# Kernel optimization log

Measured on AMD Instinct MI355X. Metric: run time of the kernel, lower is better.

## Reference

```python
import jax, jax.numpy as jnp
import numpy as np

N_WAY, K_SHOT = 5, 1
N_CLASSES = 64
D = 8


def _conv(x, w, b):
    y = jax.lax.conv_general_dilated(x, w, (2, 2), 'SAME',
                                     dimension_numbers=('NCHW', 'OIHW', 'NCHW'))
    return jax.nn.relu(y + b[None, :, None, None])


def setup_inputs() -> dict:
    key = jax.random.key(0)
    ks = jax.random.split(key, 12)
    b, s_sup, q, h, w = 4, N_WAY * K_SHOT, 1, 64, 64
    rnd = lambda k, shape: jax.random.normal(k, shape, jnp.float32) * 0.05
    return {
        'support_x': jax.random.normal(ks[0], (b, s_sup, 3, h, w), jnp.float32),
        'support_y': jax.random.randint(ks[1], (b, s_sup), 0, N_CLASSES),
        'query_x': jax.random.normal(ks[2], (b, q, 3, h, w), jnp.float32),
        'query_y': jax.random.randint(ks[3], (b, q), 0, N_CLASSES),
        'k1': rnd(ks[4], (32, 3, 3, 3)), 'bc1': jnp.zeros((32,), jnp.float32),
        'k2': rnd(ks[5], (48, 32, 3, 3)), 'bc2': jnp.zeros((48,), jnp.float32),
        'k3': rnd(ks[6], (64, 48, 3, 3)), 'bc3': jnp.zeros((64,), jnp.float32),
        'Wlog': rnd(ks[7], (64, N_CLASSES)), 'blog': jnp.zeros((N_CLASSES,), jnp.float32),
        'Wg1': rnd(ks[8], (132, 128)), 'bg1': jnp.zeros((128,), jnp.float32),
        'Wg2': rnd(ks[9], (128, 64)), 'bg2': jnp.zeros((64,), jnp.float32),
        'Wf1': rnd(ks[10], (64, 16)), 'bf1': jnp.zeros((16,), jnp.float32),
        'Wf2': rnd(ks[11], (16, 1)), 'bf2': jnp.zeros((1,), jnp.float32),
    }


def reference(support_x, support_y, query_x, query_y,
              k1, bc1, k2, bc2, k3, bc3, Wlog, blog,
              Wg1, bg1, Wg2, bg2, Wf1, bf1, Wf2, bf2):
    x = jnp.concatenate([support_x, query_x], axis=1)       # [b, s, 3, h, w]
    label = jnp.concatenate([support_y, query_y], axis=1)   # [b, s]
    b, s = label.shape
    h, w = x.shape[-2:]

    feat = x.reshape(b * s, 3, h, w)
    feat = _conv(feat, k1, bc1)
    feat = _conv(feat, k2, bc2)
    feat = _conv(feat, k3, bc3)                              # [b*s, c, D, D]
    c = feat.shape[1]
    logits = feat.mean(axis=(2, 3)) @ Wlog + blog            # [b*s, n_classes]

    # --- append normalized (i/d, j/d) coord channels ---
    ii = jnp.arange(D, dtype=feat.dtype) / D
    coord = jnp.stack([jnp.broadcast_to(ii[:, None], (D, D)),
                       jnp.broadcast_to(ii[None, :], (D, D))])        # [2, D, D]
    feat = feat.reshape(b, s, c, D, D)
    feat = jnp.concatenate([feat, jnp.broadcast_to(coord, (b, s, 2, D, D))], axis=2)
    c2 = c + 2
    m = D * D
    a = feat.reshape(b, s, c2, m).transpose(0, 1, 3, 2)      # [b, s, m, c2]

    # --- relation network g over all (set-pair, position-pair) combos ---
    # original: g(concat(x_i, x_j)) where x_i = x[b, j, :, q], x_j = x[b, i, :, p]
    # split first linear: concat @ Wg1 = x_i @ Wg1[:c2] + x_j @ Wg1[c2:]
    W1a, W1b = Wg1[:c2], Wg1[c2:]
    u = a @ W1a                                              # [b, s_j, m_q, 128]
    v = a @ W1b + bg1                                        # [b, s_i, m_p, 128]
    # hdd[b,i,j,q,p] = relu(u[b,j,q] + v[b,i,p])  -> [b, s, s, m, m, 128]
    hdd = jax.nn.relu(u[:, None, :, :, None, :] + v[:, :, None, None, :, :])
    g = jax.nn.relu(hdd @ Wg2 + bg2)                         # [b, s, s, m, m, 64]
    x_f = g.sum(axis=(3, 4))                                 # [b, s, s, 64]
    score = jax.nn.sigmoid(jax.nn.relu(x_f @ Wf1 + bf1) @ Wf2 + bf2)  # [b, s, s, 1]

    # --- losses ---
    logp = jax.nn.log_softmax(logits, axis=-1)
    lab = label.reshape(-1)
    cls_loss = -jnp.take_along_axis(logp, lab[:, None], axis=1).mean()

    y = (label[:, :, None] == label[:, None, :])[..., None].astype(score.dtype)
    P = score[..., 0]                                        # [b, s, s]
    Pt = P.transpose(0, 2, 1)
    sym, anti = 0.5 * (P + Pt), 0.5 * (P - Pt)
    sym_n = jnp.sqrt((sym ** 2).sum(axis=(1, 2)))            # Frobenius per batch
    anti_n = jnp.sqrt((anti ** 2).sum(axis=(1, 2)))
    sym_loss = ((sym_n - anti_n) / (sym_n + anti_n)).mean()
    euc_loss = ((score - y) ** 2).mean()
    rn_loss = euc_loss - 0.1 * sym_loss
    return (cls_loss, rn_loss, sym_loss)
```

## Files before the change

### kernel.cpp

```cpp
#include <hip/hip_runtime.h>

typedef _Float16 f16x8 __attribute__((ext_vector_type(8)));
typedef float f32x4 __attribute__((ext_vector_type(4)));

__device__ unsigned g_rel_done = 0;


__global__ void __launch_bounds__(256) conv1_k(
        const float* __restrict__ sx, const float* __restrict__ qx,
        const float* __restrict__ w, const float* __restrict__ bias,
        float* __restrict__ out,
        const float* __restrict__ Wg2, _Float16* __restrict__ W2h) {
    if (blockIdx.x == 768) {
        for (int s = 0; s < 4; s++) {
            int slot = threadIdx.x + 256*s;
            int tile = slot >> 6, lane = slot & 63;
            int kt = tile >> 2, nt = tile & 3;
            int quad = lane >> 4, col = lane & 15;
            f16x8 t;
            #pragma unroll
            for (int jj = 0; jj < 8; jj++)
                t[jj] = (_Float16)Wg2[(kt*32 + quad*8 + jj)*64 + nt*16 + col];
            *(f16x8*)&W2h[slot*8] = t;
        }
        return;
    }
    int r8 = blockIdx.x & 7, q = blockIdx.x >> 3;
    int n  = (q >> 5)*8 + r8;
    int oc = q & 31;
    int bi = n / 6, si = n % 6;
    const float* inp = (si < 5) ? sx + (size_t)((bi*5+si)*3)*4096
                                : qx + (size_t)(bi*3)*4096;
    __shared__ __align__(16) float ish[3*4352];
    __shared__ float wl[27];
    __shared__ float bl;
    const int tid = threadIdx.x;
    #pragma unroll
    for (int j = 0; j < 12; j++) {
        int k = tid + j*256;
        f32x4 t = *(const f32x4*)&inp[k*4];
        int plane = k >> 10, rem = k & 1023, row = rem >> 4, c4 = (rem & 15)*4;
        *(f32x4*)&ish[plane*4352 + row*68 + c4] = t;
    }
    if (tid < 27) wl[tid] = w[oc*27 + tid];
    if (tid == 31) bl = bias[oc];
    __syncthreads();
    for (int idx = tid; idx < 1024; idx += 256) {
        int oy = idx >> 5, ox = idx & 31;
        float acc = bl;
        #pragma unroll
        for (int ic = 0; ic < 3; ic++) {
            const float* ip = &ish[ic*4352];
            #pragma unroll
            for (int dy = 0; dy < 3; dy++) {
                int iy = 2*oy + dy;
                if (iy >= 64) continue;
                #pragma unroll
                for (int dx = 0; dx < 3; dx++) {
                    int ix = 2*ox + dx;
                    if (ix >= 64) continue;
                    acc += ip[iy*68+ix] * wl[ic*9 + dy*3 + dx];
                }
            }
        }
        out[(size_t)(n*32+oc)*1024 + idx] = fmaxf(acc, 0.f);
    }
}

__global__ void __launch_bounds__(256) conv2_k(
        const float* __restrict__ in, const float* __restrict__ w,
        const float* __restrict__ bias, float* __restrict__ out) {
    int r8 = blockIdx.x & 7, q = blockIdx.x >> 3;
    int n   = (q / 12)*8 + r8;
    int ocg = q % 12;
    __shared__ __align__(16) float wl[1152];
    __shared__ __align__(16) float pin[16*1152];
    const int tid = threadIdx.x;
    const float* ib = in + (size_t)n*32*1024;
    #pragma unroll
    for (int j = 0; j < 16; j++) {
        int k = tid + j*256;
        f32x4 t = *(const f32x4*)&ib[k*4];
        int s = k >> 8, rem = k & 255, row = rem >> 3, c4 = (rem & 7)*4;
        *(f32x4*)&pin[s*1152 + row*36 + c4] = t;
    }
    f32x4 rb[16];
    #pragma unroll
    for (int j = 0; j < 16; j++) {
        int k = tid + j*256;
        rb[j] = *(const f32x4*)&ib[16384 + k*4];
    }
    for (int e = tid; e < 288; e += 256)
        *(f32x4*)&wl[e*4] = *(const f32x4*)&w[ocg*1152 + e*4];
    __syncthreads();
    int oy = tid >> 4, ox = tid & 15;
    float a0 = bias[ocg*4+0], a1 = bias[ocg*4+1];
    float a2 = bias[ocg*4+2], a3 = bias[ocg*4+3];
    #pragma unroll 4
    for (int ic = 0; ic < 16; ic++) {
        const float* pp = &pin[ic*1152];
        float tap[9];
        #pragma unroll
        for (int dy = 0; dy < 3; dy++)
            #pragma unroll
            for (int dx = 0; dx < 3; dx++) {
                int iy = 2*oy+dy, ix = 2*ox+dx;
                tap[dy*3+dx] = (iy < 32 && ix < 32) ? pp[iy*36 + ix] : 0.f;
            }
        #pragma unroll
        for (int t = 0; t < 9; t++) {
            a0 += tap[t]*wl[0*288 + ic*9 + t];
            a1 += tap[t]*wl[1*288 + ic*9 + t];
            a2 += tap[t]*wl[2*288 + ic*9 + t];
            a3 += tap[t]*wl[3*288 + ic*9 + t];
        }
    }
    __syncthreads();
    #pragma unroll
    for (int j = 0; j < 16; j++) {
        int k = tid + j*256;
        int s = k >> 8, rem = k & 255, row = rem >> 3, c4 = (rem & 7)*4;
        *(f32x4*)&pin[s*1152 + row*36 + c4] = rb[j];
    }
    __syncthreads();
    #pragma unroll 4
    for (int ic = 16; ic < 32; ic++) {
        const float* pp = &pin[(ic-16)*1152];
        float tap[9];
        #pragma unroll
        for (int dy = 0; dy < 3; dy++)
            #pragma unroll
            for (int dx = 0; dx < 3; dx++) {
                int iy = 2*oy+dy, ix = 2*ox+dx;
                tap[dy*3+dx] = (iy < 32 && ix < 32) ? pp[iy*36 + ix] : 0.f;
            }
        #pragma unroll
        for (int t = 0; t < 9; t++) {
            a0 += tap[t]*wl[0*288 + ic*9 + t];
            a1 += tap[t]*wl[1*288 + ic*9 + t];
            a2 += tap[t]*wl[2*288 + ic*9 + t];
            a3 += tap[t]*wl[3*288 + ic*9 + t];
        }
    }
    size_t ob = (size_t)(n*48 + ocg*4)*256 + tid;
    out[ob        ] = fmaxf(a0, 0.f);
    out[ob + 256  ] = fmaxf(a1, 0.f);
    out[ob + 512  ] = fmaxf(a2, 0.f);
    out[ob + 768  ] = fmaxf(a3, 0.f);
}

__global__ void __launch_bounds__(256) conv3_k(
        const float* __restrict__ in, const float* __restrict__ w,
        const float* __restrict__ bias, float* __restrict__ out,
        float* __restrict__ mf) {
    int r8 = blockIdx.x & 7, q = blockIdx.x >> 3;
    int n   = (q >> 3)*8 + r8;
    int ocg = q & 7;
    __shared__ __align__(16) float wl[3456];
    __shared__ __align__(16) float pin[48*320];
    const int tid = threadIdx.x;
    const float* ib = in + (size_t)n*48*256;
    #pragma unroll
    for (int j = 0; j < 12; j++) {
        int k = tid + j*256;
        f32x4 t = *(const f32x4*)&ib[k*4];
        int plane = k >> 6, rem = k & 63, row = rem >> 2, c4 = (rem & 3)*4;
        *(f32x4*)&pin[plane*320 + row*20 + c4] = t;
    }
    for (int e = tid; e < 864; e += 256)
        *(f32x4*)&wl[e*4] = *(const f32x4*)&w[ocg*3456 + e*4];
    __syncthreads();
    int pix = tid & 63, osub = tid >> 6;
    int oy = pix >> 3, ox = pix & 7;
    int ol0 = osub*2;
    float a0 = bias[ocg*8 + ol0], a1 = bias[ocg*8 + ol0 + 1];
    #pragma unroll 4
    for (int ic = 0; ic < 48; ic++) {
        const float* pp = &pin[ic*320];
        float tap[9];
        #pragma unroll
        for (int dy = 0; dy < 3; dy++)
            #pragma unroll
            for (int dx = 0; dx < 3; dx++) {
                int iy = 2*oy+dy, ix = 2*ox+dx;
                tap[dy*3+dx] = (iy < 16 && ix < 16) ? pp[iy*20 + ix] : 0.f;
            }
        #pragma unroll
        for (int t = 0; t < 9; t++) {
            a0 += tap[t]*wl[ ol0   *432 + ic*9 + t];
            a1 += tap[t]*wl[(ol0+1)*432 + ic*9 + t];
        }
    }
    float r0 = fmaxf(a0, 0.f), r1 = fmaxf(a1, 0.f);
    out[(size_t)(n*64 + ocg*8 + ol0  )*64 + pix] = r0;
    out[(size_t)(n*64 + ocg*8 + ol0+1)*64 + pix] = r1;
    #pragma unroll
    for (int off = 32; off >= 1; off >>= 1) {
        r0 += __shfl_xor(r0, off, 64);
        r1 += __shfl_xor(r1, off, 64);
    }
    if (pix == 0) {
        mf[n*64 + ocg*8 + ol0    ] = r0 * (1.f/64.f);
        mf[n*64 + ocg*8 + ol0 + 1] = r1 * (1.f/64.f);
    }
}

__global__ void uvcls_k(const float* __restrict__ feat3, const float* __restrict__ Wg1,
                        const float* __restrict__ bg1, _Float16* __restrict__ u,
                        _Float16* __restrict__ v,
                        const float* __restrict__ mf, const int* __restrict__ sy,
                        const int* __restrict__ qy, const float* __restrict__ Wlog,
                        const float* __restrict__ blog, float* __restrict__ rv) {
    int tid = threadIdx.x;
    if (blockIdx.x >= 384) {
        int n = blockIdx.x - 384;
        if (tid >= 64) return;
        int lane = tid;
        float s = blog[lane];
        for (int c = 0; c < 64; c++) s += mf[n*64 + c] * Wlog[c*64 + lane];
        float mx = s;
        #pragma unroll
        for (int off = 32; off >= 1; off >>= 1) mx = fmaxf(mx, __shfl_xor(mx, off, 64));
        float p = __expf(s - mx);
        float se = p;
        #pragma unroll
        for (int off = 32; off >= 1; off >>= 1) se += __shfl_xor(se, off, 64);
        int bi = n/6, si = n%6;
        int lab = (si < 5) ? sy[bi*5+si] : qy[bi];
        float s_lab = __shfl(s, lab, 64);
        if (lane == 0) rv[n] = -(s_lab - mx - __logf(se));
        return;
    }
    int r8 = blockIdx.x & 7, q = blockIdx.x >> 3;
    int bs = (q >> 4)*8 + r8;
    int pg = q & 15;
    __shared__ float a4[4][66];
    for (int e = tid; e < 264; e += 128) {
        int pl = e / 66, c = e % 66;
        int p = pg*4 + pl;
        float vv;
        if (c < 64)       vv = feat3[(size_t)(bs*64 + c)*64 + p];
        else if (c == 64) vv = (float)(p >> 3) * 0.125f;
        else              vv = (float)(p & 7) * 0.125f;
        a4[pl][c] = vv;
    }
    __syncthreads();
    float us[4] = {0.f,0.f,0.f,0.f};
    float bg = bg1[tid];
    float vs[4] = {bg,bg,bg,bg};
    for (int c = 0; c < 66; c++) {
        float wa = Wg1[c*128 + tid];
        float wb = Wg1[(66+c)*128 + tid];
        #pragma unroll
        for (int pl = 0; pl < 4; pl++) {
            us[pl] += a4[pl][c]*wa;
            vs[pl] += a4[pl][c]*wb;
        }
    }
    #pragma unroll
    for (int pl = 0; pl < 4; pl++) {
        int p = pg*4 + pl;
        u[(size_t)(bs*64+p)*128 + tid] = (_Float16)us[pl];
        v[(size_t)(bs*64+p)*128 + tid] = (_Float16)vs[pl];
    }
}

__global__ void __launch_bounds__(256, 2) rel_k(
        const _Float16* __restrict__ U, const _Float16* __restrict__ V,
        const _Float16* __restrict__ W2h, const float* __restrict__ bg2,
        float* __restrict__ xfpT,
        const float* __restrict__ rv,
        const int* __restrict__ sy, const int* __restrict__ qy,
        const float* __restrict__ Wf1, const float* __restrict__ bf1,
        const float* __restrict__ Wf2, const float* __restrict__ bf2,
        float* __restrict__ out) {
    __shared__ __align__(16) float smem[1792];
    __shared__ unsigned lastflag;
    _Float16* Vsh   = (_Float16*)smem;
    float*    xfred = smem + 1024;

    int r8 = blockIdx.x & 7, qq = blockIdx.x >> 3;
    int b = r8 >> 1;
    int m = (qq << 1) | (r8 & 1);
    int cb = m >> 2, qc = m & 3;
    int j = cb / 6, i = cb % 6;
    int tid  = threadIdx.x;
    int wv   = tid >> 6, lane = tid & 63;
    int col  = lane & 15, quad = lane >> 4;

    const _Float16* ub = U + (size_t)(b*6 + i)*8192;
    const _Float16* vb = V + (size_t)(b*6 + j)*8192 + qc*16*128;

    *(f16x8*)&Vsh[tid*8] = *(const f16x8*)&vb[tid*8];

    f16x8 uf[4];
    {
        const _Float16* up = ub + (wv*16 + col)*128 + quad*8;
        #pragma unroll
        for (int kt = 0; kt < 4; kt++) uf[kt] = *(const f16x8*)&up[kt*32];
    }
    f16x8 bf[4][4];
    #pragma unroll
    for (int kt = 0; kt < 4; kt++)
        #pragma unroll
        for (int nt = 0; nt < 4; nt++)
            bf[kt][nt] = *(const f16x8*)&W2h[(size_t)(((kt*4+nt)*64) + lane)*8];
    float bgv[4];
    #pragma unroll
    for (int nt = 0; nt < 4; nt++) bgv[nt] = bg2[nt*16 + col];

    __syncthreads();

    float sums[4] = {0.f,0.f,0.f,0.f};
    for (int qi = 0; qi < 16; qi++) {
        const _Float16* vp = &Vsh[qi*128 + quad*8];
        f32x4 acc[4];
        #pragma unroll
        for (int nt = 0; nt < 4; nt++)
            acc[nt] = (f32x4){bgv[nt], bgv[nt], bgv[nt], bgv[nt]};
        #pragma unroll
        for (int kt = 0; kt < 4; kt++) {
            f16x8 vf = *(const f16x8*)&vp[kt*32];
            f16x8 af = uf[kt] + vf;
            af = __builtin_elementwise_max(af, (f16x8){0,0,0,0,0,0,0,0});
            #pragma unroll
            for (int nt = 0; nt < 4; nt++)
                acc[nt] = __builtin_amdgcn_mfma_f32_16x16x32_f16(af, bf[kt][nt], acc[nt], 0, 0, 0);
        }
        #pragma unroll
        for (int nt = 0; nt < 4; nt++)
            #pragma unroll
            for (int rr = 0; rr < 4; rr++)
                sums[nt] += fmaxf(acc[nt][rr], 0.f);
    }

    #pragma unroll
    for (int nt = 0; nt < 4; nt++) {
        sums[nt] += __shfl_xor(sums[nt], 16, 64);
        sums[nt] += __shfl_xor(sums[nt], 32, 64);
    }
    if (lane < 16) {
        #pragma unroll
        for (int nt = 0; nt < 4; nt++) xfred[wv*64 + nt*16 + lane] = sums[nt];
    }
    __syncthreads();
    if (tid < 64) {
        float val = xfred[tid] + xfred[64+tid] + xfred[128+tid] + xfred[192+tid];
        __hip_atomic_store(&xfpT[(size_t)tid*576 + (unsigned)(b*144 + m)], val,
                           __ATOMIC_RELAXED, __HIP_MEMORY_SCOPE_AGENT);
    }
    if (wv == 0) asm volatile("s_waitcnt vmcnt(0)" ::: "memory");
    if (tid == 0) {
        unsigned my = __hip_atomic_fetch_add(&g_rel_done, 1u, __ATOMIC_RELAXED,
                                             __HIP_MEMORY_SCOPE_AGENT);
        lastflag = ((my % 576u) == 575u) ? 1u : 0u;
    }
    __syncthreads();
    if (!lastflag) return;

    {
        float* Wf1sh = smem;
        float* wf2sh = smem + 1024;
        float* bf1sh = smem + 1040;
        float* Pm    = smem + 1056;
        int*   lab   = (int*)(smem + 1200);
        float* red   = smem + 1232;
        float* ratio = smem + 1488;
        for (int e = tid; e < 1024; e += 256) Wf1sh[e] = Wf1[e];
        if (tid < 16) { wf2sh[tid] = Wf2[tid]; bf1sh[tid] = bf1[tid]; }
        if (tid < 24) { int bi = tid/6, si = tid%6; lab[tid] = (si < 5) ? sy[bi*5+si] : qy[bi]; }
        __syncthreads();
        if (tid < 144) {
            float hid[16];
            #pragma unroll
            for (int h = 0; h < 16; h++) hid[h] = bf1sh[h];
            for (int nn = 0; nn < 64; nn++) {
                const float* xp = &xfpT[(size_t)nn*576 + tid*4];
                float x = 0.f;
                #pragma unroll
                for (int c = 0; c < 4; c++)
                    x += __hip_atomic_load(&xp[c], __ATOMIC_RELAXED,
                                           __HIP_MEMORY_SCOPE_AGENT);
                #pragma unroll
                for (int h = 0; h < 16; h++) hid[h] += x * Wf1sh[nn*16 + h];
            }
            float sc = bf2[0];
            #pragma unroll
            for (int h = 0; h < 16; h++) sc += fmaxf(hid[h], 0.f) * wf2sh[h];
            Pm[tid] = 1.f/(1.f + __expf(-sc));
        }
        __syncthreads();
        float e = 0.f;
        if (tid < 144) {
            int bb = tid/36, r = tid%36, jj = r/6, ii = r%6;
            float y = (lab[bb*6+jj] == lab[bb*6+ii]) ? 1.f : 0.f;
            float d = Pm[tid] - y;
            e = d*d;
        }
        red[tid] = e;
        __syncthreads();
        for (int s = 128; s > 0; s >>= 1) {
            if (tid < s) red[tid] += red[tid+s];
            __syncthreads();
        }
        if (tid < 4) {
            float s2 = 0.f, a2 = 0.f;
            for (int jj = 0; jj < 6; jj++)
                for (int ii = 0; ii < 6; ii++) {
                    float pa = Pm[tid*36 + jj*6 + ii], pb = Pm[tid*36 + ii*6 + jj];
                    float sm = 0.5f*(pa+pb), an = 0.5f*(pa-pb);
                    s2 += sm*sm; a2 += an*an;
                }
            float sn = sqrtf(s2), anq = sqrtf(a2);
            ratio[tid] = (sn - anq)/(sn + anq);
        }
        __syncthreads();
        if (tid == 0) {
            float sl = 0.25f*(ratio[0]+ratio[1]+ratio[2]+ratio[3]);
            float euc = red[0] * (1.f/144.f);
            float cs = 0.f;
            for (int k = 0; k < 24; k++) cs += rv[k];
            out[0] = cs * (1.f/24.f);
            out[1] = euc - 0.1f*sl;
            out[2] = sl;
        }
    }
}

extern "C" void kernel_launch(void* const* d_in, const int* in_sizes, int n_in,
                              void* d_out, int out_size, void* d_ws, size_t ws_size,
                              hipStream_t stream) {
    const float* sx   = (const float*)d_in[0];
    const int*   sy   = (const int*)  d_in[1];
    const float* qx   = (const float*)d_in[2];
    const int*   qy   = (const int*)  d_in[3];
    const float* k1   = (const float*)d_in[4];
    const float* bc1  = (const float*)d_in[5];
    const float* k2   = (const float*)d_in[6];
    const float* bc2  = (const float*)d_in[7];
    const float* k3   = (const float*)d_in[8];
    const float* bc3  = (const float*)d_in[9];
    const float* Wlog = (const float*)d_in[10];
    const float* blog = (const float*)d_in[11];
    const float* Wg1  = (const float*)d_in[12];
    const float* bg1  = (const float*)d_in[13];
    const float* Wg2  = (const float*)d_in[14];
    const float* bg2  = (const float*)d_in[15];
    const float* Wf1  = (const float*)d_in[16];
    const float* bf1  = (const float*)d_in[17];
    const float* Wf2  = (const float*)d_in[18];
    const float* bf2  = (const float*)d_in[19];

    float* ws    = (float*)d_ws;
    float* feat1 = ws;
    float* feat2 = feat1 + 786432;
    float* feat3 = feat2 + 294912;
    float* mf    = feat3 + 98304;
    float* rv    = mf    + 1536;
    float* xfpT  = rv    + 32;
    _Float16* u16 = (_Float16*)(xfpT + 36864);
    _Float16* v16 = u16 + 196608;
    _Float16* W2h = v16 + 196608;
    float* out   = (float*)d_out;

    conv1_k <<<769,    256, 0, stream>>>(sx, qx, k1, bc1, feat1, Wg2, W2h);
    conv2_k <<<24*12,  256, 0, stream>>>(feat1, k2, bc2, feat2);
    conv3_k <<<24*8,   256, 0, stream>>>(feat2, k3, bc3, feat3, mf);
    uvcls_k <<<408,    128, 0, stream>>>(feat3, Wg1, bg1, u16, v16,
                                         mf, sy, qy, Wlog, blog, rv);
    rel_k   <<<576,    256, 0, stream>>>(u16, v16, W2h, bg2, xfpT,
                                         rv, sy, qy, Wf1, bf1, Wf2, bf2, out);
}
```

Baseline: 162.8 us.

## Fuse conv2, conv3 and u/v projection into one kernel via last-block-per-image

Merges the conv2, conv3 and uv/classifier kernels into a single launch. Each of the 12 conv2 blocks for an image bumps a per-image atomic counter, and the last one to finish computes conv3, the mean features, the u/v projection and the classification loss for that image. This removes two kernel launches and the intermediate global round-trips between them. In exchange, conv3 and the u/v work now run serially on only 24 blocks, down from 192 and 408, which risks a long serialized tail.

```diff
diff --git a/kernel.cpp b/kernel.cpp
--- a/kernel.cpp
+++ b/kernel.cpp
@@ -4,6 +4,7 @@
 typedef float f32x4 __attribute__((ext_vector_type(4)));
 
 __device__ unsigned g_rel_done = 0;
+__device__ unsigned g_img_done[24] = {};
 
 
 __global__ void __launch_bounds__(256) conv1_k(
@@ -67,157 +68,206 @@
     }
 }
 
-__global__ void __launch_bounds__(256) conv2_k(
-        const float* __restrict__ in, const float* __restrict__ w,
-        const float* __restrict__ bias, float* __restrict__ out) {
+__global__ void __launch_bounds__(256) fused_k(
+        const float* __restrict__ feat1, const float* __restrict__ k2w,
+        const float* __restrict__ bc2, float* __restrict__ feat2,
+        const float* __restrict__ k3w, const float* __restrict__ bc3,
+        float* __restrict__ feat3g,
+        const float* __restrict__ Wg1, const float* __restrict__ bg1,
+        _Float16* __restrict__ u16, _Float16* __restrict__ v16,
+        const int* __restrict__ sy, const int* __restrict__ qy,
+        const float* __restrict__ Wlog, const float* __restrict__ blog,
+        float* __restrict__ rv) {
+    __shared__ __align__(16) float smem[19584];
+    __shared__ unsigned lastflag;
+    const int tid = threadIdx.x;
+
     int r8 = blockIdx.x & 7, q = blockIdx.x >> 3;
     int n   = (q / 12)*8 + r8;
     int ocg = q % 12;
-    __shared__ __align__(16) float wl[1152];
-    __shared__ __align__(16) float pin[16*1152];
-    const int tid = threadIdx.x;
-    const float* ib = in + (size_t)n*32*1024;
-    #pragma unroll
-    for (int j = 0; j < 16; j++) {
-        int k = tid + j*256;
-        f32x4 t = *(const f32x4*)&ib[k*4];
-        int s = k >> 8, rem = k & 255, row = rem >> 3, c4 = (rem & 7)*4;
-        *(f32x4*)&pin[s*1152 + row*36 + c4] = t;
-    }
-    f32x4 rb[16];
-    #pragma unroll
-    for (int j = 0; j < 16; j++) {
-        int k = tid + j*256;
-        rb[j] = *(const f32x4*)&ib[16384 + k*4];
-    }
-    for (int e = tid; e < 288; e += 256)
-        *(f32x4*)&wl[e*4] = *(const f32x4*)&w[ocg*1152 + e*4];
-    __syncthreads();
-    int oy = tid >> 4, ox = tid & 15;
-    float a0 = bias[ocg*4+0], a1 = bias[ocg*4+1];
-    float a2 = bias[ocg*4+2], a3 = bias[ocg*4+3];
-    #pragma unroll 4
-    for (int ic = 0; ic < 16; ic++) {
-        const float* pp = &pin[ic*1152];
-        float tap[9];
-        #pragma unroll
-        for (int dy = 0; dy < 3; dy++)
-            #pragma unroll
-            for (int dx = 0; dx < 3; dx++) {
-                int iy = 2*oy+dy, ix = 2*ox+dx;
-                tap[dy*3+dx] = (iy < 32 && ix < 32) ? pp[iy*36 + ix] : 0.f;
-            }
-        #pragma unroll
-        for (int t = 0; t < 9; t++) {
-            a0 += tap[t]*wl[0*288 + ic*9 + t];
-            a1 += tap[t]*wl[1*288 + ic*9 + t];
-            a2 += tap[t]*wl[2*288 + ic*9 + t];
-            a3 += tap[t]*wl[3*288 + ic*9 + t];
-        }
-    }
-    __syncthreads();
-    #pragma unroll
-    for (int j = 0; j < 16; j++) {
-        int k = tid + j*256;
-        int s = k >> 8, rem = k & 255, row = rem >> 3, c4 = (rem & 7)*4;
-        *(f32x4*)&pin[s*1152 + row*36 + c4] = rb[j];
-    }
-    __syncthreads();
-    #pragma unroll 4
-    for (int ic = 16; ic < 32; ic++) {
-        const float* pp = &pin[(ic-16)*1152];
-        float tap[9];
-        #pragma unroll
-        for (int dy = 0; dy < 3; dy++)
-            #pragma unroll
-            for (int dx = 0; dx < 3; dx++) {
-                int iy = 2*oy+dy, ix = 2*ox+dx;
-                tap[dy*3+dx] = (iy < 32 && ix < 32) ? pp[iy*36 + ix] : 0.f;
-            }
-        #pragma unroll
-        for (int t = 0; t < 9; t++) {
-            a0 += tap[t]*wl[0*288 + ic*9 + t];
-            a1 += tap[t]*wl[1*288 + ic*9 + t];
-            a2 += tap[t]*wl[2*288 + ic*9 + t];
-            a3 += tap[t]*wl[3*288 + ic*9 + t];
-        }
-    }
-    size_t ob = (size_t)(n*48 + ocg*4)*256 + tid;
-    out[ob        ] = fmaxf(a0, 0.f);
-    out[ob + 256  ] = fmaxf(a1, 0.f);
-    out[ob + 512  ] = fmaxf(a2, 0.f);
-    out[ob + 768  ] = fmaxf(a3, 0.f);
-}
-
-__global__ void __launch_bounds__(256) conv3_k(
-        const float* __restrict__ in, const float* __restrict__ w,
-        const float* __restrict__ bias, float* __restrict__ out,
-        float* __restrict__ mf) {
-    int r8 = blockIdx.x & 7, q = blockIdx.x >> 3;
-    int n   = (q >> 3)*8 + r8;
-    int ocg = q & 7;
-    __shared__ __align__(16) float wl[3456];
-    __shared__ __align__(16) float pin[48*320];
-    const int tid = threadIdx.x;
-    const float* ib = in + (size_t)n*48*256;
-    #pragma unroll
-    for (int j = 0; j < 12; j++) {
-        int k = tid + j*256;
-        f32x4 t = *(const f32x4*)&ib[k*4];
-        int plane = k >> 6, rem = k & 63, row = rem >> 2, c4 = (rem & 3)*4;
-        *(f32x4*)&pin[plane*320 + row*20 + c4] = t;
-    }
-    for (int e = tid; e < 864; e += 256)
-        *(f32x4*)&wl[e*4] = *(const f32x4*)&w[ocg*3456 + e*4];
-    __syncthreads();
+
+    {
+        float* wl  = smem;
+        float* pin = smem + 1152;
+        const float* ib = feat1 + (size_t)n*32*1024;
+        #pragma unroll
+        for (int j = 0; j < 16; j++) {
+            int k = tid + j*256;
+            f32x4 t = *(const f32x4*)&ib[k*4];
+            int s = k >> 8, rem = k & 255, row = rem >> 3, c4 = (rem & 7)*4;
+            *(f32x4*)&pin[s*1152 + row*36 + c4] = t;
+        }
+        f32x4 rb[16];
+        #pragma unroll
+        for (int j = 0; j < 16; j++) {
+            int k = tid + j*256;
+            rb[j] = *(const f32x4*)&ib[16384 + k*4];
+        }
+        for (int e = tid; e < 288; e += 256)
+            *(f32x4*)&wl[e*4] = *(const f32x4*)&k2w[ocg*1152 + e*4];
+        __syncthreads();
+        int oy = tid >> 4, ox = tid & 15;
+        float a0 = bc2[ocg*4+0], a1 = bc2[ocg*4+1];
+        float a2 = bc2[ocg*4+2], a3 = bc2[ocg*4+3];
+        #pragma unroll 4
+        for (int ic = 0; ic < 16; ic++) {
+            const float* pp = &pin[ic*1152];
+            float tap[9];
+            #pragma unroll
+            for (int dy = 0; dy < 3; dy++)
+                #pragma unroll
+                for (int dx = 0; dx < 3; dx++) {
+                    int iy = 2*oy+dy, ix = 2*ox+dx;
+                    tap[dy*3+dx] = (iy < 32 && ix < 32) ? pp[iy*36 + ix] : 0.f;
+                }
+            #pragma unroll
+            for (int t = 0; t < 9; t++) {
+                a0 += tap[t]*wl[0*288 + ic*9 + t];
+                a1 += tap[t]*wl[1*288 + ic*9 + t];
+                a2 += tap[t]*wl[2*288 + ic*9 + t];
+                a3 += tap[t]*wl[3*288 + ic*9 + t];
+            }
+        }
+        __syncthreads();
+        #pragma unroll
+        for (int j = 0; j < 16; j++) {
+            int k = tid + j*256;
+            int s = k >> 8, rem = k & 255, row = rem >> 3, c4 = (rem & 7)*4;
+            *(f32x4*)&pin[s*1152 + row*36 + c4] = rb[j];
+        }
+        __syncthreads();
+        #pragma unroll 4
+        for (int ic = 16; ic < 32; ic++) {
+            const float* pp = &pin[(ic-16)*1152];
+            float tap[9];
+            #pragma unroll
+            for (int dy = 0; dy < 3; dy++)
+                #pragma unroll
+                for (int dx = 0; dx < 3; dx++) {
+                    int iy = 2*oy+dy, ix = 2*ox+dx;
+                    tap[dy*3+dx] = (iy < 32 && ix < 32) ? pp[iy*36 + ix] : 0.f;
+                }
+            #pragma unroll
+            for (int t = 0; t < 9; t++) {
+                a0 += tap[t]*wl[0*288 + ic*9 + t];
+                a1 += tap[t]*wl[1*288 + ic*9 + t];
+                a2 += tap[t]*wl[2*288 + ic*9 + t];
+                a3 += tap[t]*wl[3*288 + ic*9 + t];
+            }
+        }
+        size_t ob = (size_t)(n*48 + ocg*4)*256 + tid;
+        __hip_atomic_store(&feat2[ob      ], fmaxf(a0, 0.f), __ATOMIC_RELAXED, __HIP_MEMORY_SCOPE_AGENT);
+        __hip_atomic_store(&feat2[ob + 256], fmaxf(a1, 0.f), __ATOMIC_RELAXED, __HIP_MEMORY_SCOPE_AGENT);
+        __hip_atomic_store(&feat2[ob + 512], fmaxf(a2, 0.f), __ATOMIC_RELAXED, __HIP_MEMORY_SCOPE_AGENT);
+        __hip_atomic_store(&feat2[ob + 768], fmaxf(a3, 0.f), __ATOMIC_RELAXED, __HIP_MEMORY_SCOPE_AGENT);
+    }
+    asm volatile("s_waitcnt vmcnt(0)" ::: "memory");
+    __syncthreads();
+    if (tid == 0) {
+        unsigned my = __hip_atomic_fetch_add(&g_img_done[n], 1u, __ATOMIC_RELAXED,
+                                             __HIP_MEMORY_SCOPE_AGENT);
+        lastflag = ((my % 12u) == 11u) ? 1u : 0u;
+    }
+    __syncthreads();
+    if (!lastflag) return;
+
+    float* pin3 = smem;
+    float* wl3  = smem + 15360;
+    float* mfsh = smem + 18816;
+    float* a4uv = smem + 18880;
+
+    {
+        const float* f2 = feat2 + (size_t)n*48*256;
+        #pragma unroll 8
+        for (int jj = 0; jj < 48; jj++) {
+            int k = tid + jj*256;
+            float vIn = __hip_atomic_load(&f2[k], __ATOMIC_RELAXED,
+                                          __HIP_MEMORY_SCOPE_AGENT);
+            int plane = k >> 8, rem = k & 255, row = rem >> 4, cc = rem & 15;
+            pin3[plane*320 + row*20 + cc] = vIn;
+        }
+    }
     int pix = tid & 63, osub = tid >> 6;
-    int oy = pix >> 3, ox = pix & 7;
+    int oy3 = pix >> 3, ox3 = pix & 7;
     int ol0 = osub*2;
-    float a0 = bias[ocg*8 + ol0], a1 = bias[ocg*8 + ol0 + 1];
-    #pragma unroll 4
-    for (int ic = 0; ic < 48; ic++) {
-        const float* pp = &pin[ic*320];
-        float tap[9];
-        #pragma unroll
-        for (int dy = 0; dy < 3; dy++)
-            #pragma unroll
-            for (int dx = 0; dx < 3; dx++) {
-                int iy = 2*oy+dy, ix = 2*ox+dx;
-                tap[dy*3+dx] = (iy < 16 && ix < 16) ? pp[iy*20 + ix] : 0.f;
-            }
-        #pragma unroll
-        for (int t = 0; t < 9; t++) {
-            a0 += tap[t]*wl[ ol0   *432 + ic*9 + t];
-            a1 += tap[t]*wl[(ol0+1)*432 + ic*9 + t];
-        }
-    }
-    float r0 = fmaxf(a0, 0.f), r1 = fmaxf(a1, 0.f);
-    out[(size_t)(n*64 + ocg*8 + ol0  )*64 + pix] = r0;
-    out[(size_t)(n*64 + ocg*8 + ol0+1)*64 + pix] = r1;
-    #pragma unroll
-    for (int off = 32; off >= 1; off >>= 1) {
-        r0 += __shfl_xor(r0, off, 64);
-        r1 += __shfl_xor(r1, off, 64);
-    }
-    if (pix == 0) {
-        mf[n*64 + ocg*8 + ol0    ] = r0 * (1.f/64.f);
-        mf[n*64 + ocg*8 + ol0 + 1] = r1 * (1.f/64.f);
-    }
-}
-
-__global__ void uvcls_k(const float* __restrict__ feat3, const float* __restrict__ Wg1,
-                        const float* __restrict__ bg1, _Float16* __restrict__ u,
-                        _Float16* __restrict__ v,
-                        const float* __restrict__ mf, const int* __restrict__ sy,
-                        const int* __restrict__ qy, const float* __restrict__ Wlog,
-                        const float* __restrict__ blog, float* __restrict__ rv) {
-    int tid = threadIdx.x;
-    if (blockIdx.x >= 384) {
-        int n = blockIdx.x - 384;
-        if (tid >= 64) return;
-        int lane = tid;
-        float s = blog[lane];
-        for (int c = 0; c < 64; c++) s += mf[n*64 + c] * Wlog[c*64 + lane];
+    for (int ocg3 = 0; ocg3 < 8; ocg3++) {
+        __syncthreads();
+        for (int e = tid; e < 864; e += 256)
+            *(f32x4*)&wl3[e*4] = *(const f32x4*)&k3w[ocg3*3456 + e*4];
+        __syncthreads();
+        float a0 = bc3[ocg3*8 + ol0], a1 = bc3[ocg3*8 + ol0 + 1];
+        #pragma unroll 4
+        for (int ic = 0; ic < 48; ic++) {
+            const float* pp = &pin3[ic*320];
+            float tap[9];
+            #pragma unroll
+            for (int dy = 0; dy < 3; dy++)
+                #pragma unroll
+                for (int dx = 0; dx < 3; dx++) {
+                    int iy = 2*oy3+dy, ix = 2*ox3+dx;
+                    tap[dy*3+dx] = (iy < 16 && ix < 16) ? pp[iy*20 + ix] : 0.f;
+                }
+            #pragma unroll
+            for (int t = 0; t < 9; t++) {
+                a0 += tap[t]*wl3[ ol0   *432 + ic*9 + t];
+                a1 += tap[t]*wl3[(ol0+1)*432 + ic*9 + t];
+            }
+        }
+        float r0 = fmaxf(a0, 0.f), r1 = fmaxf(a1, 0.f);
+        feat3g[(size_t)(n*64 + ocg3*8 + ol0  )*64 + pix] = r0;
+        feat3g[(size_t)(n*64 + ocg3*8 + ol0+1)*64 + pix] = r1;
+        #pragma unroll
+        for (int off = 32; off >= 1; off >>= 1) {
+            r0 += __shfl_xor(r0, off, 64);
+            r1 += __shfl_xor(r1, off, 64);
+        }
+        if (pix == 0) {
+            mfsh[ocg3*8 + ol0    ] = r0 * (1.f/64.f);
+            mfsh[ocg3*8 + ol0 + 1] = r1 * (1.f/64.f);
+        }
+    }
+    __syncthreads();
+
+    {
+        int half = tid >> 7, t = tid & 127;
+        float bg = bg1[t];
+        for (int pp2 = 0; pp2 < 8; pp2++) {
+            int pg = pp2*2 + half;
+            float* a4 = a4uv + half*264;
+            __syncthreads();
+            for (int e = t; e < 264; e += 128) {
+                int pl = e / 66, c = e % 66;
+                int p = pg*4 + pl;
+                float vv;
+                if (c < 64)       vv = feat3g[(size_t)(n*64 + c)*64 + p];
+                else if (c == 64) vv = (float)(p >> 3) * 0.125f;
+                else              vv = (float)(p & 7) * 0.125f;
+                a4[pl*66 + c] = vv;
+            }
+            __syncthreads();
+            float us[4] = {0.f,0.f,0.f,0.f};
+            float vs[4] = {bg,bg,bg,bg};
+            for (int c = 0; c < 66; c++) {
+                float wa = Wg1[c*128 + t];
+                float wb = Wg1[(66+c)*128 + t];
+                #pragma unroll
+                for (int pl = 0; pl < 4; pl++) {
+                    us[pl] += a4[pl*66 + c]*wa;
+                    vs[pl] += a4[pl*66 + c]*wb;
+                }
+            }
+            #pragma unroll
+            for (int pl = 0; pl < 4; pl++) {
+                int p = pg*4 + pl;
+                u16[(size_t)(n*64+p)*128 + t] = (_Float16)us[pl];
+                v16[(size_t)(n*64+p)*128 + t] = (_Float16)vs[pl];
+            }
+        }
+    }
+
+    if (tid < 64) {
+        float s = blog[tid];
+        for (int c = 0; c < 64; c++) s += mfsh[c] * Wlog[c*64 + tid];
         float mx = s;
         #pragma unroll
         for (int off = 32; off >= 1; off >>= 1) mx = fmaxf(mx, __shfl_xor(mx, off, 64));
@@ -228,40 +278,7 @@
         int bi = n/6, si = n%6;
         int lab = (si < 5) ? sy[bi*5+si] : qy[bi];
         float s_lab = __shfl(s, lab, 64);
-        if (lane == 0) rv[n] = -(s_lab - mx - __logf(se));
-        return;
-    }
-    int r8 = blockIdx.x & 7, q = blockIdx.x >> 3;
-    int bs = (q >> 4)*8 + r8;
-    int pg = q & 15;
-    __shared__ float a4[4][66];
-    for (int e = tid; e < 264; e += 128) {
-        int pl = e / 66, c = e % 66;
-        int p = pg*4 + pl;
-        float vv;
-        if (c < 64)       vv = feat3[(size_t)(bs*64 + c)*64 + p];
-        else if (c == 64) vv = (float)(p >> 3) * 0.125f;
-        else              vv = (float)(p & 7) * 0.125f;
-        a4[pl][c] = vv;
-    }
-    __syncthreads();
-    float us[4] = {0.f,0.f,0.f,0.f};
-    float bg = bg1[tid];
-    float vs[4] = {bg,bg,bg,bg};
-    for (int c = 0; c < 66; c++) {
-        float wa = Wg1[c*128 + tid];
-        float wb = Wg1[(66+c)*128 + tid];
-        #pragma unroll
-        for (int pl = 0; pl < 4; pl++) {
-            us[pl] += a4[pl][c]*wa;
-            vs[pl] += a4[pl][c]*wb;
-        }
-    }
-    #pragma unroll
-    for (int pl = 0; pl < 4; pl++) {
-        int p = pg*4 + pl;
-        u[(size_t)(bs*64+p)*128 + tid] = (_Float16)us[pl];
-        v[(size_t)(bs*64+p)*128 + tid] = (_Float16)vs[pl];
+        if (tid == 0) rv[n] = -(s_lab - mx - __logf(se));
     }
 }
 
@@ -463,11 +480,9 @@
     _Float16* W2h = v16 + 196608;
     float* out   = (float*)d_out;
 
-    conv1_k <<<769,    256, 0, stream>>>(sx, qx, k1, bc1, feat1, Wg2, W2h);
-    conv2_k <<<24*12,  256, 0, stream>>>(feat1, k2, bc2, feat2);
-    conv3_k <<<24*8,   256, 0, stream>>>(feat2, k3, bc3, feat3, mf);
-    uvcls_k <<<408,    128, 0, stream>>>(feat3, Wg1, bg1, u16, v16,
-                                         mf, sy, qy, Wlog, blog, rv);
-    rel_k   <<<576,    256, 0, stream>>>(u16, v16, W2h, bg2, xfpT,
-                                         rv, sy, qy, Wf1, bf1, Wf2, bf2, out);
+    conv1_k <<<769,   256, 0, stream>>>(sx, qx, k1, bc1, feat1, Wg2, W2h);
+    fused_k <<<24*12, 256, 0, stream>>>(feat1, k2, bc2, feat2, k3, bc3, feat3,
+                                        Wg1, bg1, u16, v16, sy, qy, Wlog, blog, rv);
+    rel_k   <<<576,   256, 0, stream>>>(u16, v16, W2h, bg2, xfpT,
+                                        rv, sy, qy, Wf1, bf1, Wf2, bf2, out);
 }
```

After: 279.5 us. 71.7% more time.
